# Kernel optimization log

Hardware: AMD Instinct MI355X
Metric: run time of the kernel (lower is better)

The kernel has to match this reference:

```python
import jax, jax.numpy as jnp
import numpy as np

B, S, D = 2, 2048, 1024
H, HD = 16, 64
INIT = 0.02

def setup_inputs() -> dict:
    key = jax.random.key(0)
    k1, k2, k3 = jax.random.split(key, 3)
    x = jax.random.normal(k1, (B, S, D), dtype=jnp.float32)
    w_attn = jax.random.normal(k2, (D, 3 * D), dtype=jnp.float32) * INIT
    b_attn = jnp.zeros((3 * D,), dtype=jnp.float32)
    w_proj = jax.random.normal(k3, (D, D), dtype=jnp.float32) * INIT
    b_proj = jnp.zeros((D,), dtype=jnp.float32)
    return {"x": x, "w_attn": w_attn, "b_attn": b_attn, "w_proj": w_proj, "b_proj": b_proj}

def reference(x, w_attn, b_attn, w_proj, b_proj):
    # c_attn: [B,S,D] -> [B,S,3D]
    hidden = jnp.einsum('bse,ef->bsf', x, w_attn) + b_attn
    q, k, v = jnp.split(hidden, 3, axis=-1)
    # split heads -> [B,S,H,HD]
    q = q.reshape(B, S, H, HD) / jnp.sqrt(jnp.float32(HD))
    k = k.reshape(B, S, H, HD)
    v = v.reshape(B, S, H, HD)
    # scores: [B,H,S,S]
    scores = jnp.einsum('bqhd,bkhd->bhqk', q, k)
    causal = jnp.tril(jnp.ones((S, S), dtype=bool))  # [S,S]
    big_neg = jnp.finfo(jnp.float32).min
    scores = jnp.where(causal[None, None, :, :], scores, big_neg)
    weights = jax.nn.softmax(scores, axis=-1)
    z = jnp.einsum('bhqk,bkhd->bqhd', weights, v)
    merged = z.reshape(B, S, D)
    out = jnp.einsum('bse,ef->bsf', merged, w_proj) + b_proj
    return out
```

## Files before the change

### kernel.cpp

```cpp
#include <hip/hip_runtime.h>
#include <hip/hip_bf16.h>

typedef __attribute__((ext_vector_type(8))) short bf16x8;
typedef __attribute__((ext_vector_type(4))) float f32x4;
typedef unsigned short u16;
typedef unsigned int u32;

#define B_ 2
#define S_ 2048
#define D_ 1024
#define H_ 16
#define HD_ 64

#define LOG2E 1.44269504088896340736f
#define M0 4.0f

__device__ __forceinline__ u16 f2bf(float f) {
    __hip_bfloat16 h = __float2bfloat16(f);
    u16 r;
    __builtin_memcpy(&r, &h, 2);
    return r;
}

__device__ __forceinline__ float ex2(float x) {
    float r;
    asm("v_exp_f32 %0, %1" : "=v"(r) : "v"(x));
    return r;
}

__device__ __forceinline__ void gload16(const u16* gsrc, u16* lds_base) {
    __builtin_amdgcn_global_load_lds(
        (const __attribute__((address_space(1))) void*)gsrc,
        (__attribute__((address_space(3))) void*)lds_base, 16, 0, 0);
}

__device__ __forceinline__ bf16x8 rd64(const u16* lds, int row, int c) {
    return *(const bf16x8*)&lds[row * 64 + (c ^ ((row & 7) * 8))];
}

__global__ __launch_bounds__(256) void cvt_bf16(const float* __restrict__ in,
                                                u16* __restrict__ out) {
    int i = blockIdx.x * 256 + threadIdx.x;
    float4 v = ((const float4*)in)[i];
    ushort4 o;
    o.x = f2bf(v.x); o.y = f2bf(v.y); o.z = f2bf(v.z); o.w = f2bf(v.w);
    ((ushort4*)out)[i] = o;
}

__global__ __launch_bounds__(256) void tconv(const float* __restrict__ in,
                                             u16* __restrict__ out, int R, int C) {
    __shared__ float t[32][33];
    int c0 = blockIdx.x * 32, r0 = blockIdx.y * 32;
    int lx = threadIdx.x & 31, ly = threadIdx.x >> 5;
#pragma unroll
    for (int i = 0; i < 4; ++i)
        t[ly + i * 8][lx] = in[(size_t)(r0 + ly + i * 8) * C + c0 + lx];
    __syncthreads();
#pragma unroll
    for (int i = 0; i < 4; ++i)
        out[(size_t)(c0 + ly + i * 8) * R + r0 + lx] = f2bf(t[lx][ly + i * 8]);
}

__global__ __launch_bounds__(512, 1) void gemm192(
    const u16* __restrict__ A, const u16* __restrict__ Bt,
    const float* __restrict__ bias,
    u16* __restrict__ oQ, u16* __restrict__ oK, u16* __restrict__ oV) {
    extern __shared__ u16 lds[];
    u16* Al[2] = {lds, lds + 16384};
    u16* Bl[2] = {lds + 32768, lds + 32768 + 12288};

    const int tid = threadIdx.x;
    const int lane = tid & 63, w = tid >> 6;
    const int wm = w >> 2, wn = w & 3;
    const int l15 = lane & 15, lg = lane >> 4;
    const int lin = blockIdx.y * 16 + blockIdx.x;
    const int nl = (lin & 7) * 32 + (lin >> 3);
    const int m0 = (nl >> 4) * 256, n0 = (nl & 15) * 192;

    const int lrow = lane >> 3;
    const int csrc = ((lane & 7) * 8) ^ ((lrow & 7) * 8);
    const u16* pA = A + (size_t)(m0 + w * 32 + lrow) * 1024 + csrc;
    const u16* pB = Bt + (size_t)(n0 + w * 24 + lrow) * 1024 + csrc;

    const int sw8 = (l15 & 7) * 8;
    const int c0 = (lg * 8) ^ sw8;
    const int c1 = (32 + lg * 8) ^ sw8;
    const int abase = (wm * 128 + l15) * 64;
    const int bbase = (wn * 48 + l15) * 64;

    f32x4 acc[8][3] = {};
    bf16x8 afr[4][2], bfr[3][2];

#define STGA(bb, tt) { \
    _Pragma("unroll") for (int i_ = 0; i_ < 4; ++i_) \
        gload16(pA + (size_t)(tt) * 64 + i_ * 8192, Al[bb] + w * 2048 + i_ * 512); }
#define STGB(bb, tt) { \
    _Pragma("unroll") for (int j_ = 0; j_ < 3; ++j_) \
        gload16(pB + (size_t)(tt) * 64 + j_ * 8192, Bl[bb] + w * 1536 + j_ * 512); }

#define RDA(bb, AH) \
    _Pragma("unroll") for (int mt_ = 0; mt_ < 4; ++mt_) { \
        afr[mt_][0] = *(const bf16x8*)&Al[bb][abase + (AH) * 4096 + mt_ * 1024 + c0]; \
        afr[mt_][1] = *(const bf16x8*)&Al[bb][abase + (AH) * 4096 + mt_ * 1024 + c1]; }

#define RDB(bb) \
    _Pragma("unroll") for (int nt_ = 0; nt_ < 3; ++nt_) { \
        bfr[nt_][0] = *(const bf16x8*)&Bl[bb][bbase + nt_ * 1024 + c0]; \
        bfr[nt_][1] = *(const bf16x8*)&Bl[bb][bbase + nt_ * 1024 + c1]; }

#define MFMA24(AH) \
    __builtin_amdgcn_s_setprio(1); \
    _Pragma("unroll") for (int mt_ = 0; mt_ < 4; ++mt_) \
    _Pragma("unroll") for (int nt_ = 0; nt_ < 3; ++nt_) { \
        acc[(AH)*4+mt_][nt_] = __builtin_amdgcn_mfma_f32_16x16x32_bf16( \
            afr[mt_][0], bfr[nt_][0], acc[(AH)*4+mt_][nt_], 0, 0, 0); \
        acc[(AH)*4+mt_][nt_] = __builtin_amdgcn_mfma_f32_16x16x32_bf16( \
            afr[mt_][1], bfr[nt_][1], acc[(AH)*4+mt_][nt_], 0, 0, 0); } \
    __builtin_amdgcn_s_setprio(0);

#define BAR __builtin_amdgcn_s_barrier();
#define VMC3 { asm volatile("s_waitcnt vmcnt(3)" ::: "memory"); __builtin_amdgcn_sched_barrier(0); }
#define VMC0 { asm volatile("s_waitcnt vmcnt(0)" ::: "memory"); __builtin_amdgcn_sched_barrier(0); }

    STGB(0, 0); STGA(0, 0); STGB(1, 1);
    VMC3; BAR;

#pragma unroll 1
    for (int t = 0; t < 8; ++t) {
        const bool nf = (t < 7);
        RDA(0, 0) RDB(0)
        STGA(1, 2 * t + 1);
        BAR; MFMA24(0) BAR;
        RDA(0, 1)
        if (nf) STGB(0, 2 * t + 2);
        BAR; MFMA24(1)
        if (nf) { VMC3 } else { VMC0 }
        BAR;
        RDA(1, 0) RDB(1)
        if (nf) STGA(0, 2 * t + 2);
        BAR; MFMA24(0) BAR;
        RDA(1, 1)
        if (nf) STGB(1, 2 * t + 3);
        BAR; MFMA24(1)
        if (nf) { VMC3 }
        BAR;
    }

#pragma unroll
    for (int mt = 0; mt < 8; ++mt) {
#pragma unroll
        for (int nt = 0; nt < 3; ++nt) {
            const int n_g = n0 + wn * 48 + nt * 16 + l15;
            const int m_b = m0 + wm * 128 + mt * 16 + lg * 4;
            const float bs = bias[n_g];
            const int which = n_g >> 10;
            const int nn = n_g & 1023;
            const int h = nn >> 6, hd = nn & 63;
            const int bb = m_b >> 11, s = m_b & 2047;
            if (which == 2) {
                ushort4 pv;
                pv.x = f2bf(acc[mt][nt][0] + bs);
                pv.y = f2bf(acc[mt][nt][1] + bs);
                pv.z = f2bf(acc[mt][nt][2] + bs);
                pv.w = f2bf(acc[mt][nt][3] + bs);
                *(ushort4*)&oV[((size_t)(bb * H_ + h) * HD_ + hd) * S_ + s] = pv;
            } else {
                u16* dst = which == 0 ? oQ : oK;
                const float scale = which == 0 ? (0.125f * LOG2E) : 1.0f;
#pragma unroll
                for (int r = 0; r < 4; ++r)
                    dst[((size_t)(bb * H_ + h) * S_ + s + r) * HD_ + hd] =
                        f2bf((acc[mt][nt][r] + bs) * scale);
            }
        }
    }
#undef STGA
#undef STGB
#undef RDA
#undef RDB
#undef MFMA24
#undef BAR
#undef VMC3
#undef VMC0
}

__global__ __launch_bounds__(256) void gemm_bt2(
    const u16* __restrict__ A, const u16* __restrict__ Bt,
    const float* __restrict__ bias, float* __restrict__ oF) {
    __shared__ u16 Al[64 * 64];
    __shared__ u16 Bl[128 * 64];
    const int tid = threadIdx.x;
    const int lane = tid & 63, w = tid >> 6;
    const int wm = w >> 1, wn = w & 1;
    const int l15 = lane & 15, lg = lane >> 4;
    const int lin = blockIdx.y * 8 + blockIdx.x;
    const int nl = (lin & 7) * 64 + (lin >> 3);
    const int m0 = (nl >> 3) * 64, n0 = (nl & 7) * 128;
    f32x4 acc[2][4] = {};
    const int lrow = lane >> 3;
    const int csrc = ((lane & 7) * 8) ^ ((lrow & 7) * 8);

    for (int k0 = 0; k0 < 1024; k0 += 64) {
        __syncthreads();
        const u16* ga = A + (size_t)m0 * 1024 + k0;
        const u16* gb = Bt + (size_t)n0 * 1024 + k0;
#pragma unroll
        for (int i = 0; i < 2; ++i) {
            const int j = w * 2 + i;
            gload16(ga + (size_t)(j * 8 + lrow) * 1024 + csrc, &Al[j * 512]);
        }
#pragma unroll
        for (int i = 0; i < 4; ++i) {
            const int j = w * 4 + i;
            gload16(gb + (size_t)(j * 8 + lrow) * 1024 + csrc, &Bl[j * 512]);
        }
        __syncthreads();
#pragma unroll
        for (int g = 0; g < 2; ++g) {
            bf16x8 af[2], bfr[4];
#pragma unroll
            for (int t = 0; t < 2; ++t)
                af[t] = rd64(Al, wm * 32 + t * 16 + l15, g * 32 + lg * 8);
#pragma unroll
            for (int t = 0; t < 4; ++t)
                bfr[t] = rd64(Bl, wn * 64 + t * 16 + l15, g * 32 + lg * 8);
#pragma unroll
            for (int mt = 0; mt < 2; ++mt)
#pragma unroll
                for (int nt = 0; nt < 4; ++nt)
                    acc[mt][nt] = __builtin_amdgcn_mfma_f32_16x16x32_bf16(
                        af[mt], bfr[nt], acc[mt][nt], 0, 0, 0);
        }
    }
#pragma unroll
    for (int mt = 0; mt < 2; ++mt)
#pragma unroll
        for (int nt = 0; nt < 4; ++nt) {
            const int n_g = n0 + wn * 64 + nt * 16 + l15;
            const int m_b = m0 + wm * 32 + mt * 16 + lg * 4;
            const float bs = bias[n_g];
#pragma unroll
            for (int r = 0; r < 4; ++r)
                oF[(size_t)(m_b + r) * 1024 + n_g] = acc[mt][nt][r] + bs;
        }
}

__global__ __launch_bounds__(256, 2) void attn7(
    const u16* __restrict__ Q, const u16* __restrict__ Kp,
    const u16* __restrict__ VT, u16* __restrict__ Om) {
    extern __shared__ u16 lds[];
    u16* Kl = lds;
    u16* Vl = lds + 16384;
    u16* Pl = lds + 32768;
    const int tid = threadIdx.x;
    const int lane = tid & 63, w = tid >> 6;
    const int l15 = lane & 15, lg = lane >> 4;
    const int hw = blockIdx.x;
    const int bid = (hw & 7) * 64 + (hw >> 3);
    const int bh = bid >> 4, p = bid & 15;
    const int b = bh >> 4, h = bh & 15;
    const size_t baseK = (size_t)bh * (S_ * HD_);
    const u16* gk = Kp + baseK;
    const u16* gv = VT + (size_t)bh * (HD_ * S_);

    const int lrow = lane >> 3;
    const int csK = ((lane & 7) * 8) ^ ((lrow & 7) * 8);
    const int lg2 = lane >> 4;
    const int csV0 = ((lane & 15) * 8) ^ (lg2 * 8);
    const int csV1 = ((lane & 15) * 8) ^ ((4 + lg2) * 8);
    const u16* gkp[4];
    const u16* gvp[4];
#pragma unroll
    for (int i = 0; i < 4; ++i) {
        gkp[i] = gk + (size_t)(w * 32 + i * 8 + lrow) * HD_ + csK;
        gvp[i] = gv + (size_t)(w * 16 + i * 4 + lg2) * S_ + ((i & 1) ? csV1 : csV0);
    }
    u16* ldsK = Kl + w * 2048;
    u16* ldsV = Vl + w * 2048;

    const int sw = (l15 & 7) * 8;
    const int roK0 = l15 * 128 + 2 * ((lg * 8) ^ sw);
    const int roK1 = l15 * 128 + 2 * ((32 + lg * 8) ^ sw);
    int po[4];
#pragma unroll
    for (int g = 0; g < 4; ++g) po[g] = 2 * ((g * 32 + lg * 8) ^ sw);
    const char* kbase = (const char*)Kl;
    const char* vbase = (const char*)Vl;
    char* plw = (char*)(Pl + w * 2048);
    const int prb = l15 * 256;
    int pwo[8];
#pragma unroll
    for (int nt = 0; nt < 8; ++nt) pwo[nt] = prb + 2 * ((nt * 16 + lg * 4) ^ sw);

#pragma unroll 1
    for (int t = 0; t < 2; ++t) {
        const int qb = t == 0 ? (31 - p) : p;
        const int q0 = qb * 64 + w * 16;
        const int qg = q0 + l15;
        const int kiters = (qb + 2) >> 1;

        const bf16x8 qf0 = *(const bf16x8*)&Q[baseK + (size_t)qg * HD_ + lg * 8];
        const bf16x8 qf1 = *(const bf16x8*)&Q[baseK + (size_t)qg * HD_ + 32 + lg * 8];

        f32x4 acc[4] = {};
        float l_run = 0.0f;

        __syncthreads();
#pragma unroll
        for (int i = 0; i < 4; ++i) {
            gload16(gkp[i], ldsK + i * 512);
            gload16(gvp[i], ldsV + i * 512);
        }

        for (int it = 0; it < kiters; ++it) {
            const int cur = it & 1;
            const int bo = cur * 16384;
            __syncthreads();
            if (it + 1 < kiters) {
                const int be = (cur ^ 1) * 8192;
                const int kt2 = (it + 1) * 128;
#pragma unroll
                for (int i = 0; i < 4; ++i) {
                    gload16(gkp[i] + kt2 * HD_, ldsK + be + i * 512);
                    gload16(gvp[i] + kt2, ldsV + be + i * 512);
                }
            }
            const char* kb = kbase + bo;
            f32x4 sc[8];
            __builtin_amdgcn_s_setprio(1);
#pragma unroll
            for (int nt = 0; nt < 8; ++nt) {
                bf16x8 kf = *(const bf16x8*)(kb + nt * 2048 + roK0);
                sc[nt] = __builtin_amdgcn_mfma_f32_16x16x32_bf16(kf, qf0, f32x4{}, 0, 0, 0);
            }
#pragma unroll
            for (int nt = 0; nt < 8; ++nt) {
                bf16x8 kf = *(const bf16x8*)(kb + nt * 2048 + roK1);
                sc[nt] = __builtin_amdgcn_mfma_f32_16x16x32_bf16(kf, qf1, sc[nt], 0, 0, 0);
            }
            __builtin_amdgcn_s_setprio(0);
            if (it == kiters - 1) {
                const int tcmp = qg - it * 128;
#pragma unroll
                for (int nt = 0; nt < 8; ++nt)
#pragma unroll
                    for (int r = 0; r < 4; ++r)
                        if (nt * 16 + lg * 4 + r > tcmp) sc[nt][r] = -1e30f;
            }
            float ps = 0.0f;
#pragma unroll
            for (int nt = 0; nt < 8; ++nt) {
                float a = ex2(sc[nt][0] - M0);
                float c = ex2(sc[nt][1] - M0);
                float d = ex2(sc[nt][2] - M0);
                float e = ex2(sc[nt][3] - M0);
                sc[nt][0] = a; sc[nt][1] = c; sc[nt][2] = d; sc[nt][3] = e;
                ps += (a + c) + (d + e);
            }
            l_run += ps;
#pragma unroll
            for (int nt = 0; nt < 8; ++nt) {
                ushort4 pk;
                pk.x = f2bf(sc[nt][0]); pk.y = f2bf(sc[nt][1]);
                pk.z = f2bf(sc[nt][2]); pk.w = f2bf(sc[nt][3]);
                *(ushort4*)(plw + pwo[nt]) = pk;
            }
            const char* vb = vbase + bo;
            __builtin_amdgcn_s_setprio(1);
#pragma unroll
            for (int g = 0; g < 4; ++g) {
                bf16x8 pb = *(const bf16x8*)(plw + prb + po[g]);
#pragma unroll
                for (int dt = 0; dt < 4; ++dt) {
                    bf16x8 vf = *(const bf16x8*)(vb + (dt * 16 + l15) * 256 + po[g]);
                    acc[dt] = __builtin_amdgcn_mfma_f32_16x16x32_bf16(vf, pb, acc[dt], 0, 0, 0);
                }
            }
            __builtin_amdgcn_s_setprio(0);
        }
        float lt = l_run + __shfl_xor(l_run, 16, 64);
        lt = lt + __shfl_xor(lt, 32, 64);
        const float rl = 1.0f / lt;
#pragma unroll
        for (int dt = 0; dt < 4; ++dt) {
            ushort4 ov;
            ov.x = f2bf(acc[dt][0] * rl);
            ov.y = f2bf(acc[dt][1] * rl);
            ov.z = f2bf(acc[dt][2] * rl);
            ov.w = f2bf(acc[dt][3] * rl);
            *(ushort4*)&Om[((size_t)b * S_ + qg) * D_ + h * HD_ + dt * 16 + lg * 4] = ov;
        }
    }
}

extern "C" void kernel_launch(void* const* d_in, const int* in_sizes, int n_in,
                              void* d_out, int out_size, void* d_ws, size_t ws_size,
                              hipStream_t stream) {
    const float* x      = (const float*)d_in[0];
    const float* w_attn = (const float*)d_in[1];
    const float* b_attn = (const float*)d_in[2];
    const float* w_proj = (const float*)d_in[3];
    const float* b_proj = (const float*)d_in[4];
    float* out = (float*)d_out;

    char* ws = (char*)d_ws;
    const size_t XE = (size_t)B_ * S_ * D_;
    u16* x_bf = (u16*)ws;            ws += XE * 2;
    u16* waT  = (u16*)ws;            ws += (size_t)3 * D_ * D_ * 2;
    u16* wpT  = (u16*)ws;            ws += (size_t)D_ * D_ * 2;
    u16* Qb   = (u16*)ws;            ws += XE * 2;
    u16* Kb   = (u16*)ws;            ws += XE * 2;
    u16* Vt   = (u16*)ws;            ws += XE * 2;
    u16* Mg   = x_bf;

    hipFuncSetAttribute((const void*)gemm192,
                        hipFuncAttributeMaxDynamicSharedMemorySize, 114688);
    hipFuncSetAttribute((const void*)attn7,
                        hipFuncAttributeMaxDynamicSharedMemorySize, 81920);

    cvt_bf16<<<(int)(XE / 4 / 256), 256, 0, stream>>>(x, x_bf);
    tconv<<<dim3(3 * D_ / 32, D_ / 32), 256, 0, stream>>>(w_attn, waT, D_, 3 * D_);
    tconv<<<dim3(D_ / 32, D_ / 32), 256, 0, stream>>>(w_proj, wpT, D_, D_);

    gemm192<<<dim3(16, 16), 512, 114688, stream>>>(x_bf, waT, b_attn, Qb, Kb, Vt);

    attn7<<<B_ * H_ * 16, 256, 81920, stream>>>(Qb, Kb, Vt, Mg);

    gemm_bt2<<<dim3(8, 64), 256, 0, stream>>>(Mg, wpT, b_proj, out);
}
```

Before: 100.3 us.

## Share K/V tile loads across paired query blocks and fuse prep kernels

The attention kernel used to process its two causal-balanced query blocks one after the other, loading K/V tiles twice. It now interleaves both query blocks in a single loop, so each K/V tile is loaded once and reused for block B while block B still needs it. This cuts global traffic and barriers in exchange for more registers (two accumulator sets and two Q fragments), which may reduce occupancy. The three preprocessing kernels (x conversion and two weight transposes) are also merged into one launch to cut launch overhead.

```diff
diff --git a/kernel.cpp b/kernel.cpp
--- a/kernel.cpp
+++ b/kernel.cpp
@@ -38,20 +38,35 @@
     return *(const bf16x8*)&lds[row * 64 + (c ^ ((row & 7) * 8))];
 }
 
-__global__ __launch_bounds__(256) void cvt_bf16(const float* __restrict__ in,
-                                                u16* __restrict__ out) {
-    int i = blockIdx.x * 256 + threadIdx.x;
-    float4 v = ((const float4*)in)[i];
-    ushort4 o;
-    o.x = f2bf(v.x); o.y = f2bf(v.y); o.z = f2bf(v.z); o.w = f2bf(v.w);
-    ((ushort4*)out)[i] = o;
-}
-
-__global__ __launch_bounds__(256) void tconv(const float* __restrict__ in,
-                                             u16* __restrict__ out, int R, int C) {
+__global__ __launch_bounds__(256) void prep(
+    const float* __restrict__ x, u16* __restrict__ x_bf,
+    const float* __restrict__ wa, u16* __restrict__ waT,
+    const float* __restrict__ wp, u16* __restrict__ wpT) {
     __shared__ float t[32][33];
-    int c0 = blockIdx.x * 32, r0 = blockIdx.y * 32;
-    int lx = threadIdx.x & 31, ly = threadIdx.x >> 5;
+    const int bid = blockIdx.x;
+    const int tid = threadIdx.x;
+    if (bid < 4096) {
+        int i = bid * 256 + tid;
+        float4 v = ((const float4*)x)[i];
+        ushort4 o;
+        o.x = f2bf(v.x); o.y = f2bf(v.y); o.z = f2bf(v.z); o.w = f2bf(v.w);
+        ((ushort4*)x_bf)[i] = o;
+        return;
+    }
+    const float* in;
+    u16* out;
+    int R = 1024, C, bx, by;
+    if (bid < 4096 + 3072) {
+        in = wa; out = waT; C = 3072;
+        int idx = bid - 4096;
+        bx = idx % 96; by = idx / 96;
+    } else {
+        in = wp; out = wpT; C = 1024;
+        int idx = bid - 7168;
+        bx = idx % 32; by = idx / 32;
+    }
+    const int c0 = bx * 32, r0 = by * 32;
+    const int lx = tid & 31, ly = tid >> 5;
 #pragma unroll
     for (int i = 0; i < 4; ++i)
         t[ly + i * 8][lx] = in[(size_t)(r0 + ly + i * 8) * C + c0 + lx];
@@ -245,7 +260,7 @@
         }
 }
 
-__global__ __launch_bounds__(256, 2) void attn7(
+__global__ __launch_bounds__(256, 2) void attn8(
     const u16* __restrict__ Q, const u16* __restrict__ Kp,
     const u16* __restrict__ VT, u16* __restrict__ Om) {
     extern __shared__ u16 lds[];
@@ -292,103 +307,135 @@
 #pragma unroll
     for (int nt = 0; nt < 8; ++nt) pwo[nt] = prb + 2 * ((nt * 16 + lg * 4) ^ sw);
 
-#pragma unroll 1
-    for (int t = 0; t < 2; ++t) {
-        const int qb = t == 0 ? (31 - p) : p;
-        const int q0 = qb * 64 + w * 16;
-        const int qg = q0 + l15;
-        const int kiters = (qb + 2) >> 1;
-
-        const bf16x8 qf0 = *(const bf16x8*)&Q[baseK + (size_t)qg * HD_ + lg * 8];
-        const bf16x8 qf1 = *(const bf16x8*)&Q[baseK + (size_t)qg * HD_ + 32 + lg * 8];
-
-        f32x4 acc[4] = {};
-        float l_run = 0.0f;
-
+    const int qbA = 31 - p, qbB = p;
+    const int kitA = (qbA + 2) >> 1, kitB = (qbB + 2) >> 1;
+    const int qgA = qbA * 64 + w * 16 + l15;
+    const int qgB = qbB * 64 + w * 16 + l15;
+
+    const bf16x8 qa0 = *(const bf16x8*)&Q[baseK + (size_t)qgA * HD_ + lg * 8];
+    const bf16x8 qa1 = *(const bf16x8*)&Q[baseK + (size_t)qgA * HD_ + 32 + lg * 8];
+    const bf16x8 qb0 = *(const bf16x8*)&Q[baseK + (size_t)qgB * HD_ + lg * 8];
+    const bf16x8 qb1 = *(const bf16x8*)&Q[baseK + (size_t)qgB * HD_ + 32 + lg * 8];
+
+    f32x4 accA[4] = {}, accB[4] = {};
+    float lA = 0.0f, lB = 0.0f;
+
+#pragma unroll
+    for (int i = 0; i < 4; ++i) {
+        gload16(gkp[i], ldsK + i * 512);
+        gload16(gvp[i], ldsV + i * 512);
+    }
+
+#define QK8(sc, q0v, q1v) { \
+    _Pragma("unroll") for (int nt_ = 0; nt_ < 8; ++nt_) { \
+        bf16x8 kf = *(const bf16x8*)(kb + nt_ * 2048 + roK0); \
+        sc[nt_] = __builtin_amdgcn_mfma_f32_16x16x32_bf16(kf, q0v, f32x4{}, 0, 0, 0); } \
+    _Pragma("unroll") for (int nt_ = 0; nt_ < 8; ++nt_) { \
+        bf16x8 kf = *(const bf16x8*)(kb + nt_ * 2048 + roK1); \
+        sc[nt_] = __builtin_amdgcn_mfma_f32_16x16x32_bf16(kf, q1v, sc[nt_], 0, 0, 0); } }
+
+#define SMFIX(sc, lrun) { \
+    float ps_ = 0.0f; \
+    _Pragma("unroll") for (int nt_ = 0; nt_ < 8; ++nt_) { \
+        float a_ = ex2(sc[nt_][0] - M0); \
+        float c_ = ex2(sc[nt_][1] - M0); \
+        float d_ = ex2(sc[nt_][2] - M0); \
+        float e_ = ex2(sc[nt_][3] - M0); \
+        sc[nt_][0] = a_; sc[nt_][1] = c_; sc[nt_][2] = d_; sc[nt_][3] = e_; \
+        ps_ += (a_ + c_) + (d_ + e_); } \
+    lrun += ps_; }
+
+#define PWR(sc) { \
+    _Pragma("unroll") for (int nt_ = 0; nt_ < 8; ++nt_) { \
+        ushort4 pk_; \
+        pk_.x = f2bf(sc[nt_][0]); pk_.y = f2bf(sc[nt_][1]); \
+        pk_.z = f2bf(sc[nt_][2]); pk_.w = f2bf(sc[nt_][3]); \
+        *(ushort4*)(plw + pwo[nt_]) = pk_; } }
+
+#define PV8(accv) { \
+    _Pragma("unroll") for (int g_ = 0; g_ < 4; ++g_) { \
+        bf16x8 pb_ = *(const bf16x8*)(plw + prb + po[g_]); \
+        _Pragma("unroll") for (int dt_ = 0; dt_ < 4; ++dt_) { \
+            bf16x8 vf_ = *(const bf16x8*)(vb + (dt_ * 16 + l15) * 256 + po[g_]); \
+            accv[dt_] = __builtin_amdgcn_mfma_f32_16x16x32_bf16(vf_, pb_, accv[dt_], 0, 0, 0); } } }
+
+#define MASK8(sc, tc) { \
+    _Pragma("unroll") for (int nt_ = 0; nt_ < 8; ++nt_) \
+    _Pragma("unroll") for (int r_ = 0; r_ < 4; ++r_) \
+        if (nt_ * 16 + lg * 4 + r_ > (tc)) sc[nt_][r_] = -1e30f; }
+
+    for (int it = 0; it < kitA; ++it) {
+        const int cur = it & 1;
+        const int bo = cur * 16384;
         __syncthreads();
-#pragma unroll
-        for (int i = 0; i < 4; ++i) {
-            gload16(gkp[i], ldsK + i * 512);
-            gload16(gvp[i], ldsV + i * 512);
-        }
-
-        for (int it = 0; it < kiters; ++it) {
-            const int cur = it & 1;
-            const int bo = cur * 16384;
-            __syncthreads();
-            if (it + 1 < kiters) {
-                const int be = (cur ^ 1) * 8192;
-                const int kt2 = (it + 1) * 128;
-#pragma unroll
-                for (int i = 0; i < 4; ++i) {
-                    gload16(gkp[i] + kt2 * HD_, ldsK + be + i * 512);
-                    gload16(gvp[i] + kt2, ldsV + be + i * 512);
-                }
+        if (it + 1 < kitA) {
+            const int be = (cur ^ 1) * 8192;
+            const int kt2 = (it + 1) * 128;
+#pragma unroll
+            for (int i = 0; i < 4; ++i) {
+                gload16(gkp[i] + kt2 * HD_, ldsK + be + i * 512);
+                gload16(gvp[i] + kt2, ldsV + be + i * 512);
             }
-            const char* kb = kbase + bo;
+        }
+        const char* kb = kbase + bo;
+        const char* vb = vbase + bo;
+        {
             f32x4 sc[8];
             __builtin_amdgcn_s_setprio(1);
-#pragma unroll
-            for (int nt = 0; nt < 8; ++nt) {
-                bf16x8 kf = *(const bf16x8*)(kb + nt * 2048 + roK0);
-                sc[nt] = __builtin_amdgcn_mfma_f32_16x16x32_bf16(kf, qf0, f32x4{}, 0, 0, 0);
-            }
-#pragma unroll
-            for (int nt = 0; nt < 8; ++nt) {
-                bf16x8 kf = *(const bf16x8*)(kb + nt * 2048 + roK1);
-                sc[nt] = __builtin_amdgcn_mfma_f32_16x16x32_bf16(kf, qf1, sc[nt], 0, 0, 0);
-            }
+            QK8(sc, qa0, qa1)
             __builtin_amdgcn_s_setprio(0);
-            if (it == kiters - 1) {
-                const int tcmp = qg - it * 128;
-#pragma unroll
-                for (int nt = 0; nt < 8; ++nt)
-#pragma unroll
-                    for (int r = 0; r < 4; ++r)
-                        if (nt * 16 + lg * 4 + r > tcmp) sc[nt][r] = -1e30f;
-            }
-            float ps = 0.0f;
-#pragma unroll
-            for (int nt = 0; nt < 8; ++nt) {
-                float a = ex2(sc[nt][0] - M0);
-                float c = ex2(sc[nt][1] - M0);
-                float d = ex2(sc[nt][2] - M0);
-                float e = ex2(sc[nt][3] - M0);
-                sc[nt][0] = a; sc[nt][1] = c; sc[nt][2] = d; sc[nt][3] = e;
-                ps += (a + c) + (d + e);
-            }
-            l_run += ps;
-#pragma unroll
-            for (int nt = 0; nt < 8; ++nt) {
-                ushort4 pk;
-                pk.x = f2bf(sc[nt][0]); pk.y = f2bf(sc[nt][1]);
-                pk.z = f2bf(sc[nt][2]); pk.w = f2bf(sc[nt][3]);
-                *(ushort4*)(plw + pwo[nt]) = pk;
-            }
-            const char* vb = vbase + bo;
+            if (it == kitA - 1) MASK8(sc, qgA - it * 128)
+            SMFIX(sc, lA)
+            PWR(sc)
             __builtin_amdgcn_s_setprio(1);
-#pragma unroll
-            for (int g = 0; g < 4; ++g) {
-                bf16x8 pb = *(const bf16x8*)(plw + prb + po[g]);
-#pragma unroll
-                for (int dt = 0; dt < 4; ++dt) {
-                    bf16x8 vf = *(const bf16x8*)(vb + (dt * 16 + l15) * 256 + po[g]);
-                    acc[dt] = __builtin_amdgcn_mfma_f32_16x16x32_bf16(vf, pb, acc[dt], 0, 0, 0);
-                }
-            }
+            PV8(accA)
             __builtin_amdgcn_s_setprio(0);
         }
-        float lt = l_run + __shfl_xor(l_run, 16, 64);
+        if (it < kitB) {
+            f32x4 sc[8];
+            __builtin_amdgcn_s_setprio(1);
+            QK8(sc, qb0, qb1)
+            __builtin_amdgcn_s_setprio(0);
+            if (it == kitB - 1) MASK8(sc, qgB - it * 128)
+            SMFIX(sc, lB)
+            PWR(sc)
+            __builtin_amdgcn_s_setprio(1);
+            PV8(accB)
+            __builtin_amdgcn_s_setprio(0);
+        }
+    }
+#undef QK8
+#undef SMFIX
+#undef PWR
+#undef PV8
+#undef MASK8
+
+    {
+        float lt = lA + __shfl_xor(lA, 16, 64);
         lt = lt + __shfl_xor(lt, 32, 64);
         const float rl = 1.0f / lt;
 #pragma unroll
         for (int dt = 0; dt < 4; ++dt) {
             ushort4 ov;
-            ov.x = f2bf(acc[dt][0] * rl);
-            ov.y = f2bf(acc[dt][1] * rl);
-            ov.z = f2bf(acc[dt][2] * rl);
-            ov.w = f2bf(acc[dt][3] * rl);
-            *(ushort4*)&Om[((size_t)b * S_ + qg) * D_ + h * HD_ + dt * 16 + lg * 4] = ov;
+            ov.x = f2bf(accA[dt][0] * rl);
+            ov.y = f2bf(accA[dt][1] * rl);
+            ov.z = f2bf(accA[dt][2] * rl);
+            ov.w = f2bf(accA[dt][3] * rl);
+            *(ushort4*)&Om[((size_t)b * S_ + qgA) * D_ + h * HD_ + dt * 16 + lg * 4] = ov;
+        }
+    }
+    {
+        float lt = lB + __shfl_xor(lB, 16, 64);
+        lt = lt + __shfl_xor(lt, 32, 64);
+        const float rl = 1.0f / lt;
+#pragma unroll
+        for (int dt = 0; dt < 4; ++dt) {
+            ushort4 ov;
+            ov.x = f2bf(accB[dt][0] * rl);
+            ov.y = f2bf(accB[dt][1] * rl);
+            ov.z = f2bf(accB[dt][2] * rl);
+            ov.w = f2bf(accB[dt][3] * rl);
+            *(ushort4*)&Om[((size_t)b * S_ + qgB) * D_ + h * HD_ + dt * 16 + lg * 4] = ov;
         }
     }
 }
@@ -415,16 +462,14 @@
 
     hipFuncSetAttribute((const void*)gemm192,
                         hipFuncAttributeMaxDynamicSharedMemorySize, 114688);
-    hipFuncSetAttribute((const void*)attn7,
+    hipFuncSetAttribute((const void*)attn8,
                         hipFuncAttributeMaxDynamicSharedMemorySize, 81920);
 
-    cvt_bf16<<<(int)(XE / 4 / 256), 256, 0, stream>>>(x, x_bf);
-    tconv<<<dim3(3 * D_ / 32, D_ / 32), 256, 0, stream>>>(w_attn, waT, D_, 3 * D_);
-    tconv<<<dim3(D_ / 32, D_ / 32), 256, 0, stream>>>(w_proj, wpT, D_, D_);
+    prep<<<8192, 256, 0, stream>>>(x, x_bf, w_attn, waT, w_proj, wpT);
 
     gemm192<<<dim3(16, 16), 512, 114688, stream>>>(x_bf, waT, b_attn, Qb, Kb, Vt);
 
-    attn7<<<B_ * H_ * 16, 256, 81920, stream>>>(Qb, Kb, Vt, Mg);
+    attn8<<<B_ * H_ * 16, 256, 81920, stream>>>(Qb, Kb, Vt, Mg);
 
     gemm_bt2<<<dim3(8, 64), 256, 0, stream>>>(Mg, wpT, b_proj, out);
 }
```

Result: faster. 94.60 us (-5.7%).
